# Kernel tuning notes

Hardware: AMD Instinct MI355X
Metric: run time of the kernel (lower is better)

## Reference

```python
import jax, jax.numpy as jnp
import numpy as np

DIM = 256
NUM_HEADS = 8
HEAD_DIM = DIM // NUM_HEADS
WH, WW = 7, 7
N = WH * WW              # tokens per window = 49
NUM_WINDOWS = 64         # windows per image (56x56 map / 7x7 windows)
B_TOTAL = 2048           # num_windows * B_images
SCALE = HEAD_DIM ** -0.5


def _relative_position_index():
    # Matches the tf.meshgrid (xy indexing) construction in the source.
    coords = np.stack(np.meshgrid(np.arange(WH), np.arange(WW)), axis=0)  # [2, WW, WH]
    flat = coords.reshape(2, -1)                                          # [2, N]
    rel = flat[:, :, None] - flat[:, None, :]                             # [2, N, N]
    rel = rel.transpose(1, 2, 0).astype(np.int32)                         # [N, N, 2]
    rel[:, :, 0] += WH - 1
    rel[:, :, 1] += WW - 1
    rel[:, :, 0] *= 2 * WW - 1
    return rel.sum(-1)                                                    # [N, N]


def setup_inputs() -> dict:
    key = jax.random.key(0)
    ks = jax.random.split(key, 6)
    std = 0.02
    x = jax.random.normal(ks[0], (B_TOTAL, N, DIM), dtype=jnp.float32)
    mask = jnp.zeros((NUM_WINDOWS, N, N), dtype=jnp.float32)  # 0 / -inf additive mask
    qkv_w = jax.random.normal(ks[1], (DIM, 3 * DIM), dtype=jnp.float32) * std
    qkv_b = jnp.zeros((3 * DIM,), dtype=jnp.float32)
    proj_w = jax.random.normal(ks[2], (DIM, DIM), dtype=jnp.float32) * std
    proj_b = jnp.zeros((DIM,), dtype=jnp.float32)
    n_rel = (2 * WH - 1) * (2 * WW - 1)  # 169
    bias_table = jax.random.normal(ks[3], (n_rel, NUM_HEADS), dtype=jnp.float32) * std
    rel_index = jnp.asarray(_relative_position_index(), dtype=jnp.int32)
    return {"x": x, "mask": mask, "qkv_w": qkv_w, "qkv_b": qkv_b,
            "proj_w": proj_w, "proj_b": proj_b, "bias_table": bias_table,
            "rel_index": rel_index}


def reference(x, mask, qkv_w, qkv_b, proj_w, proj_b, bias_table, rel_index):
    B = x.shape[0]
    # qkv projection -> [3, B, H, N, hd]
    qkv = x @ qkv_w + qkv_b                                  # [B, N, 3C]
    qkv = qkv.reshape(B, N, 3, NUM_HEADS, HEAD_DIM)
    qkv = jnp.transpose(qkv, (2, 0, 3, 1, 4))
    q, k, v = qkv[0], qkv[1], qkv[2]
    # scaled attention scores [B, H, N, N]
    attn = jnp.einsum('bhnd,bhmd->bhnm', q, k) * SCALE
    # relative position bias gather: [N*N] -> [N, N, H] -> [1, H, N, N]
    bias = bias_table[rel_index.reshape(-1)].reshape(N, N, NUM_HEADS)
    attn = attn + jnp.transpose(bias, (2, 0, 1))[None]
    # additive window mask [nW, N, N]
    nW = mask.shape[0]
    attn = attn.reshape(B // nW, nW, NUM_HEADS, N, N) + mask[None, :, None]
    attn = attn.reshape(B, NUM_HEADS, N, N)
    attn = jax.nn.softmax(attn, axis=-1)
    out = jnp.einsum('bhnm,bhmd->bhnd', attn, v)             # [B, H, N, hd]
    out = jnp.transpose(out, (0, 2, 1, 3)).reshape(B, N, DIM)
    return out @ proj_w + proj_b
```

## Files before the change

### kernel.cpp

```cpp
#include <hip/hip_runtime.h>

#define NTOK 49
#define NHEAD 8
#define HDIM 32
#define DIMC 256
#define SCALE_F 0.17677669529663687f

typedef __attribute__((ext_vector_type(8))) short short8;
typedef __attribute__((ext_vector_type(4))) float f32x4;

#define AS1P(p) ((__attribute__((address_space(1))) void*)(p))
#define AS3P(p) ((__attribute__((address_space(3))) void*)(p))

__device__ inline unsigned short f2bf(float f) {
    unsigned int u = __float_as_uint(f);
    u += 0x7fffu + ((u >> 16) & 1u);
    return (unsigned short)(u >> 16);
}

__global__ __launch_bounds__(256) void conv_bf16(const float* __restrict__ in,
    unsigned short* __restrict__ outp, int nv8)
{
    int i = blockIdx.x * 256 + threadIdx.x;
    if (i >= nv8) return;
    const float4* p = (const float4*)in + (size_t)i * 2;
    float4 a = p[0], b = p[1];
    union { unsigned short s[8]; uint4 v; } u;
    u.s[0] = f2bf(a.x); u.s[1] = f2bf(a.y); u.s[2] = f2bf(a.z); u.s[3] = f2bf(a.w);
    u.s[4] = f2bf(b.x); u.s[5] = f2bf(b.y); u.s[6] = f2bf(b.z); u.s[7] = f2bf(b.w);
    ((uint4*)outp)[i] = u.v;
}

__global__ __launch_bounds__(256) void pack_w(const float* __restrict__ W,
    unsigned short* __restrict__ Wp, int K, int N)
{
    int idx = blockIdx.x * 256 + threadIdx.x;
    if (idx >= K * N) return;
    int k = idx / N, n = idx - k * N;
    Wp[((size_t)(k >> 3) * N + n) * 8 + (k & 7)] = f2bf(W[idx]);
}

__global__ __launch_bounds__(256) void bm_build(const float* __restrict__ bias_table,
    const int* __restrict__ rel_index, const float* __restrict__ mask,
    float* __restrict__ bm)
{
    int idx = blockIdx.x * 256 + threadIdx.x;
    if (idx >= 64 * NHEAD * NTOK * NTOK) return;
    int wh = idx / (NTOK * NTOK);
    int ij = idx - wh * (NTOK * NTOK);
    int w = wh >> 3, h = wh & 7;
    bm[idx] = bias_table[rel_index[ij] * NHEAD + h] + mask[(size_t)w * (NTOK * NTOK) + ij];
}

template <bool OUT_BF16>
__global__ __launch_bounds__(256) void gemm_mfma(
    const unsigned short* __restrict__ A,
    const unsigned short* __restrict__ Wp,
    const float* __restrict__ Bv,
    void* __restrict__ Yv,
    int N)
{
    __shared__ __align__(16) unsigned short As[4096];
    __shared__ __align__(16) unsigned short Bs[4096];

    const int tid  = threadIdx.x;
    const int lane = tid & 63;
    const int wv   = tid >> 6;
    const int quad = lane >> 4;
    const int l15  = lane & 15;
    const long m0  = (long)blockIdx.y * 128;
    const int  n0  = blockIdx.x * 128;
    const int  wm  = (wv >> 1) * 64;
    const int  wn  = (wv & 1) * 64;

    const unsigned short* ga0 = A + (size_t)(m0 + lane) * 256 + wv * 8;
    const unsigned short* ga1 = A + (size_t)(m0 + 64 + lane) * 256 + wv * 8;
    const unsigned short* gb0 = Wp + ((size_t)wv * N + n0 + lane) * 8;
    const unsigned short* gb1 = Wp + ((size_t)wv * N + n0 + 64 + lane) * 8;

    f32x4 acc[4][4];
    #pragma unroll
    for (int i = 0; i < 4; ++i)
        #pragma unroll
        for (int j = 0; j < 4; ++j) acc[i][j] = (f32x4){0.f, 0.f, 0.f, 0.f};

    for (int k0 = 0; k0 < 256; k0 += 32) {
        const size_t bofs = (size_t)(k0 >> 3) * N * 8;
        __builtin_amdgcn_global_load_lds(AS1P(ga0 + k0),   AS3P(As + wv * 1024),       16, 0, 0);
        __builtin_amdgcn_global_load_lds(AS1P(ga1 + k0),   AS3P(As + wv * 1024 + 512), 16, 0, 0);
        __builtin_amdgcn_global_load_lds(AS1P(gb0 + bofs), AS3P(Bs + wv * 1024),       16, 0, 0);
        __builtin_amdgcn_global_load_lds(AS1P(gb1 + bofs), AS3P(Bs + wv * 1024 + 512), 16, 0, 0);
        __syncthreads();
        short8 af[4], bq[4];
        #pragma unroll
        for (int t = 0; t < 4; ++t) {
            af[t] = *(const short8*)(As + quad * 1024 + (wm + t * 16 + l15) * 8);
            bq[t] = *(const short8*)(Bs + quad * 1024 + (wn + t * 16 + l15) * 8);
        }
        #pragma unroll
        for (int ti = 0; ti < 4; ++ti)
            #pragma unroll
            for (int tj = 0; tj < 4; ++tj)
                acc[ti][tj] = __builtin_amdgcn_mfma_f32_16x16x32_bf16(af[ti], bq[tj], acc[ti][tj], 0, 0, 0);
        __syncthreads();
    }

    #pragma unroll
    for (int ti = 0; ti < 4; ++ti) {
        #pragma unroll
        for (int r = 0; r < 4; ++r) {
            const long row = m0 + wm + ti * 16 + quad * 4 + r;
            #pragma unroll
            for (int tj = 0; tj < 4; ++tj) {
                const int col = n0 + wn + tj * 16 + l15;
                float v = acc[ti][tj][r] + Bv[col];
                if (OUT_BF16) ((unsigned short*)Yv)[row * N + col] = f2bf(v);
                else          ((float*)Yv)[row * N + col] = v;
            }
        }
    }
}

__global__ __launch_bounds__(128) void attn_mfma(
    const unsigned short* __restrict__ qkvb,
    const float* __restrict__ bm,
    unsigned short* __restrict__ o1b,
    int win0)
{
    __shared__ __align__(16) unsigned short SMEM[2 * 3528];

    const int wvid = threadIdx.x >> 6;
    const int lane = threadIdx.x & 63;
    const int h    = blockIdx.x * 2 + wvid;
    const int b    = blockIdx.y;
    const int w    = (win0 + b) & 63;
    const int quad = lane >> 4;
    const int l15  = lane & 15;

    unsigned short* Vt = SMEM + wvid * 3528;
    unsigned short* Ps = SMEM + wvid * 3528;

    const unsigned short* wbase = qkvb + (size_t)b * NTOK * 768 + h * HDIM;

    {
        const int tok = (lane < NTOK) ? lane : (NTOK - 1);
        const unsigned short* vp = wbase + (size_t)tok * 768 + 512;
        #pragma unroll
        for (int c = 0; c < 4; ++c) {
            uint4 vv = *(const uint4*)(vp + c * 8);
            unsigned int uu[4] = {vv.x, vv.y, vv.z, vv.w};
            #pragma unroll
            for (int e = 0; e < 4; ++e) {
                int d = c * 8 + e * 2;
                Vt[d * 72 + lane]       = (unsigned short)(uu[e] & 0xffffu);
                Vt[(d + 1) * 72 + lane] = (unsigned short)(uu[e] >> 16);
            }
        }
    }

    short8 aq[4], bk[4];
    #pragma unroll
    for (int t = 0; t < 4; ++t) {
        int row = t * 16 + l15; if (row >= NTOK) row = NTOK - 1;
        const unsigned short* rp = wbase + (size_t)row * 768 + quad * 8;
        aq[t] = *(const short8*)(rp);
        bk[t] = *(const short8*)(rp + 256);
    }

    f32x4 sa[4][4];
    #pragma unroll
    for (int ti = 0; ti < 4; ++ti)
        #pragma unroll
        for (int tj = 0; tj < 4; ++tj) {
            f32x4 z = (f32x4){0.f, 0.f, 0.f, 0.f};
            sa[ti][tj] = __builtin_amdgcn_mfma_f32_16x16x32_bf16(aq[ti], bk[tj], z, 0, 0, 0);
        }

    short8 vb2[2][2];
    #pragma unroll
    for (int td = 0; td < 2; ++td)
        #pragma unroll
        for (int kc = 0; kc < 2; ++kc)
            vb2[td][kc] = *(const short8*)(Vt + (td * 16 + l15) * 72 + kc * 32 + quad * 8);

    const float* bmb = bm + (size_t)(w * NHEAD + h) * (NTOK * NTOK);
    float inv[4][4];
    #pragma unroll
    for (int ti = 0; ti < 4; ++ti) {
        #pragma unroll
        for (int r = 0; r < 4; ++r) {
            const int row = ti * 16 + quad * 4 + r;
            float sv[4];
            #pragma unroll
            for (int tj = 0; tj < 4; ++tj) {
                const int col = tj * 16 + l15;
                float s;
                if (col < NTOK) {
                    float add = (row < NTOK) ? bmb[row * NTOK + col] : 0.f;
                    s = sa[ti][tj][r] * SCALE_F + add;
                } else {
                    s = -__builtin_inff();
                }
                sv[tj] = s;
            }
            float mx = fmaxf(fmaxf(sv[0], sv[1]), fmaxf(sv[2], sv[3]));
            mx = fmaxf(mx, __shfl_xor(mx, 1, 16));
            mx = fmaxf(mx, __shfl_xor(mx, 2, 16));
            mx = fmaxf(mx, __shfl_xor(mx, 4, 16));
            mx = fmaxf(mx, __shfl_xor(mx, 8, 16));
            float e0 = __expf(sv[0] - mx), e1 = __expf(sv[1] - mx);
            float e2 = __expf(sv[2] - mx), e3 = __expf(sv[3] - mx);
            sa[ti][0][r] = e0; sa[ti][1][r] = e1; sa[ti][2][r] = e2; sa[ti][3][r] = e3;
            float sum = (e0 + e1) + (e2 + e3);
            sum += __shfl_xor(sum, 1, 16);
            sum += __shfl_xor(sum, 2, 16);
            sum += __shfl_xor(sum, 4, 16);
            sum += __shfl_xor(sum, 8, 16);
            inv[ti][r] = 1.f / sum;
        }
    }

    __syncthreads();

    #pragma unroll
    for (int ti = 0; ti < 4; ++ti)
        #pragma unroll
        for (int r = 0; r < 4; ++r) {
            const int row = ti * 16 + quad * 4 + r;
            if (row < NTOK) {
                #pragma unroll
                for (int tj = 0; tj < 4; ++tj)
                    Ps[row * 72 + tj * 16 + l15] = f2bf(sa[ti][tj][r]);
            }
        }

    short8 pa[4][2];
    #pragma unroll
    for (int ti = 0; ti < 4; ++ti) {
        int row = ti * 16 + l15; if (row >= NTOK) row = NTOK - 1;
        #pragma unroll
        for (int kc = 0; kc < 2; ++kc)
            pa[ti][kc] = *(const short8*)(Ps + row * 72 + kc * 32 + quad * 8);
    }
    f32x4 oa[4][2];
    #pragma unroll
    for (int ti = 0; ti < 4; ++ti)
        #pragma unroll
        for (int td = 0; td < 2; ++td) {
            f32x4 z = (f32x4){0.f, 0.f, 0.f, 0.f};
            z = __builtin_amdgcn_mfma_f32_16x16x32_bf16(pa[ti][0], vb2[td][0], z, 0, 0, 0);
            oa[ti][td] = __builtin_amdgcn_mfma_f32_16x16x32_bf16(pa[ti][1], vb2[td][1], z, 0, 0, 0);
        }

    #pragma unroll
    for (int ti = 0; ti < 4; ++ti)
        #pragma unroll
        for (int r = 0; r < 4; ++r) {
            const int row = ti * 16 + quad * 4 + r;
            if (row < NTOK) {
                const float si = inv[ti][r];
                unsigned short* op = o1b + ((size_t)b * NTOK + row) * DIMC + h * HDIM;
                #pragma unroll
                for (int td = 0; td < 2; ++td)
                    op[td * 16 + l15] = f2bf(oa[ti][td][r] * si);
            }
        }
}

extern "C" void kernel_launch(void* const* d_in, const int* in_sizes, int n_in,
                              void* d_out, int out_size, void* d_ws, size_t ws_size,
                              hipStream_t stream)
{
    const float* x          = (const float*)d_in[0];
    const float* mask       = (const float*)d_in[1];
    const float* qkv_w      = (const float*)d_in[2];
    const float* qkv_b      = (const float*)d_in[3];
    const float* proj_w     = (const float*)d_in[4];
    const float* proj_b     = (const float*)d_in[5];
    const float* bias_table = (const float*)d_in[6];
    const int*   rel_index  = (const int*)d_in[7];
    float* outp = (float*)d_out;

    const int B_TOTAL = 2048;
    char* ws = (char*)d_ws;
    size_t off = 0;
    auto carve = [&](size_t bytes) -> void* {
        void* p = ws + off; off += (bytes + 255) & ~(size_t)255; return p;
    };
    unsigned short* WpQ = (unsigned short*)carve((size_t)256 * 768 * 2);
    unsigned short* WpP = (unsigned short*)carve((size_t)256 * 256 * 2);
    float* bm = (float*)carve((size_t)64 * NHEAD * NTOK * NTOK * 4);
    const size_t fixed = off;
    const size_t PER_WIN = (size_t)NTOK * 256 * 2 + (size_t)NTOK * 768 * 2 + (size_t)NTOK * 256 * 2;
    size_t avail = (ws_size > fixed + 1024) ? (ws_size - fixed - 1024) : 0;
    int chunkW = (int)(avail / PER_WIN);
    if (chunkW > B_TOTAL) chunkW = B_TOTAL;
    chunkW &= ~127;
    if (chunkW < 128) chunkW = 128;
    unsigned short* x_bf = (unsigned short*)carve((size_t)chunkW * NTOK * 256 * 2);
    unsigned short* qkvb = (unsigned short*)carve((size_t)chunkW * NTOK * 768 * 2);
    unsigned short* o1b  = (unsigned short*)carve((size_t)chunkW * NTOK * 256 * 2);

    pack_w<<<(256 * 768 + 255) / 256, 256, 0, stream>>>(qkv_w, WpQ, 256, 768);
    pack_w<<<(256 * 256 + 255) / 256, 256, 0, stream>>>(proj_w, WpP, 256, 256);
    bm_build<<<(64 * NHEAD * NTOK * NTOK + 255) / 256, 256, 0, stream>>>(
        bias_table, rel_index, mask, bm);

    for (int w0 = 0; w0 < B_TOTAL; w0 += chunkW) {
        int wc = B_TOTAL - w0; if (wc > chunkW) wc = chunkW;
        const int Mc = wc * NTOK;
        const int nv8 = Mc * 32;
        conv_bf16<<<(nv8 + 255) / 256, 256, 0, stream>>>(
            x + (size_t)w0 * NTOK * DIMC, x_bf, nv8);
        gemm_mfma<true ><<<dim3(6, Mc / 128), 256, 0, stream>>>(x_bf, WpQ, qkv_b, qkvb, 768);
        attn_mfma<<<dim3(NHEAD / 2, wc), 128, 0, stream>>>(qkvb, bm, o1b, w0);
        gemm_mfma<false><<<dim3(2, Mc / 128), 256, 0, stream>>>(
            o1b, WpP, proj_b, outp + (size_t)w0 * NTOK * DIMC, 256);
    }
}
```

Baseline: 400.0 us.

## Pack activations k-major, swap MFMA operands for vector stores, XCD-aware block mapping

The bf16 activation buffers (x and the attention output) are now written in a k-chunk-major packed layout, the same one the weights use, so the GEMM's global-to-LDS A loads are contiguous per lane instead of 512-byte strided. The MFMA operands are swapped so each lane holds four consecutive output columns, which lets the epilogue issue float4/uint2 vector stores and load the bias as float4. The GEMM grid is flattened and remapped so each XCD works on a contiguous range of M blocks, aiming for better L2 locality. The attention kernel now writes its output with scattered 2-byte stores into the packed layout, which may cost more than the contiguous row writes it replaces.

After: 413.9 us. 1.03x slower.

```diff
diff --git a/kernel.cpp b/kernel.cpp
--- a/kernel.cpp
+++ b/kernel.cpp
@@ -18,17 +18,18 @@
     return (unsigned short)(u >> 16);
 }
 
-__global__ __launch_bounds__(256) void conv_bf16(const float* __restrict__ in,
-    unsigned short* __restrict__ outp, int nv8)
-{
-    int i = blockIdx.x * 256 + threadIdx.x;
-    if (i >= nv8) return;
-    const float4* p = (const float4*)in + (size_t)i * 2;
+__global__ __launch_bounds__(256) void conv_pack(const float* __restrict__ in,
+    unsigned short* __restrict__ xp, int M)
+{
+    const int m  = blockIdx.x * 256 + threadIdx.x;
+    const int kc = blockIdx.y;
+    if (m >= M) return;
+    const float4* p = (const float4*)(in + (size_t)m * 256 + kc * 8);
     float4 a = p[0], b = p[1];
     union { unsigned short s[8]; uint4 v; } u;
     u.s[0] = f2bf(a.x); u.s[1] = f2bf(a.y); u.s[2] = f2bf(a.z); u.s[3] = f2bf(a.w);
     u.s[4] = f2bf(b.x); u.s[5] = f2bf(b.y); u.s[6] = f2bf(b.z); u.s[7] = f2bf(b.w);
-    ((uint4*)outp)[i] = u.v;
+    *(uint4*)(xp + ((size_t)kc * M + m) * 8) = u.v;
 }
 
 __global__ __launch_bounds__(256) void pack_w(const float* __restrict__ W,
@@ -54,11 +55,11 @@
 
 template <bool OUT_BF16>
 __global__ __launch_bounds__(256) void gemm_mfma(
-    const unsigned short* __restrict__ A,
+    const unsigned short* __restrict__ Ap,
     const unsigned short* __restrict__ Wp,
     const float* __restrict__ Bv,
     void* __restrict__ Yv,
-    int N)
+    int N, int M, int nbm)
 {
     __shared__ __align__(16) unsigned short As[4096];
     __shared__ __align__(16) unsigned short Bs[4096];
@@ -68,15 +69,29 @@
     const int wv   = tid >> 6;
     const int quad = lane >> 4;
     const int l15  = lane & 15;
-    const long m0  = (long)blockIdx.y * 128;
-    const int  n0  = blockIdx.x * 128;
-    const int  wm  = (wv >> 1) * 64;
-    const int  wn  = (wv & 1) * 64;
-
-    const unsigned short* ga0 = A + (size_t)(m0 + lane) * 256 + wv * 8;
-    const unsigned short* ga1 = A + (size_t)(m0 + 64 + lane) * 256 + wv * 8;
+
+    const int nbn = N >> 7;
+    const int lin = blockIdx.x;
+    int mblk, nblk;
+    if ((nbm & 7) == 0) {
+        const int xcd = lin & 7;
+        const int g   = lin >> 3;
+        const int gm  = g / nbn;
+        mblk = xcd * (nbm >> 3) + gm;
+        nblk = g - gm * nbn;
+    } else {
+        mblk = lin / nbn;
+        nblk = lin - mblk * nbn;
+    }
+    const long m0 = (long)mblk * 128;
+    const int  n0 = nblk * 128;
+    const int  wm = (wv >> 1) * 64;
+    const int  wn = (wv & 1) * 64;
+
+    const unsigned short* ga0 = Ap + ((size_t)wv * M + m0 + lane) * 8;
+    const unsigned short* ga1 = ga0 + 64 * 8;
     const unsigned short* gb0 = Wp + ((size_t)wv * N + n0 + lane) * 8;
-    const unsigned short* gb1 = Wp + ((size_t)wv * N + n0 + 64 + lane) * 8;
+    const unsigned short* gb1 = gb0 + 64 * 8;
 
     f32x4 acc[4][4];
     #pragma unroll
@@ -85,9 +100,10 @@
         for (int j = 0; j < 4; ++j) acc[i][j] = (f32x4){0.f, 0.f, 0.f, 0.f};
 
     for (int k0 = 0; k0 < 256; k0 += 32) {
+        const size_t aofs = (size_t)(k0 >> 3) * M * 8;
         const size_t bofs = (size_t)(k0 >> 3) * N * 8;
-        __builtin_amdgcn_global_load_lds(AS1P(ga0 + k0),   AS3P(As + wv * 1024),       16, 0, 0);
-        __builtin_amdgcn_global_load_lds(AS1P(ga1 + k0),   AS3P(As + wv * 1024 + 512), 16, 0, 0);
+        __builtin_amdgcn_global_load_lds(AS1P(ga0 + aofs), AS3P(As + wv * 1024),       16, 0, 0);
+        __builtin_amdgcn_global_load_lds(AS1P(ga1 + aofs), AS3P(As + wv * 1024 + 512), 16, 0, 0);
         __builtin_amdgcn_global_load_lds(AS1P(gb0 + bofs), AS3P(Bs + wv * 1024),       16, 0, 0);
         __builtin_amdgcn_global_load_lds(AS1P(gb1 + bofs), AS3P(Bs + wv * 1024 + 512), 16, 0, 0);
         __syncthreads();
@@ -101,21 +117,33 @@
         for (int ti = 0; ti < 4; ++ti)
             #pragma unroll
             for (int tj = 0; tj < 4; ++tj)
-                acc[ti][tj] = __builtin_amdgcn_mfma_f32_16x16x32_bf16(af[ti], bq[tj], acc[ti][tj], 0, 0, 0);
+                acc[ti][tj] = __builtin_amdgcn_mfma_f32_16x16x32_bf16(bq[tj], af[ti], acc[ti][tj], 0, 0, 0);
         __syncthreads();
     }
 
+    float4 bv4[4];
+    #pragma unroll
+    for (int tj = 0; tj < 4; ++tj)
+        bv4[tj] = *(const float4*)(Bv + n0 + wn + tj * 16 + quad * 4);
+
     #pragma unroll
     for (int ti = 0; ti < 4; ++ti) {
-        #pragma unroll
-        for (int r = 0; r < 4; ++r) {
-            const long row = m0 + wm + ti * 16 + quad * 4 + r;
-            #pragma unroll
-            for (int tj = 0; tj < 4; ++tj) {
-                const int col = n0 + wn + tj * 16 + l15;
-                float v = acc[ti][tj][r] + Bv[col];
-                if (OUT_BF16) ((unsigned short*)Yv)[row * N + col] = f2bf(v);
-                else          ((float*)Yv)[row * N + col] = v;
+        const long row = m0 + wm + ti * 16 + l15;
+        #pragma unroll
+        for (int tj = 0; tj < 4; ++tj) {
+            const int col = n0 + wn + tj * 16 + quad * 4;
+            const float v0 = acc[ti][tj][0] + bv4[tj].x;
+            const float v1 = acc[ti][tj][1] + bv4[tj].y;
+            const float v2 = acc[ti][tj][2] + bv4[tj].z;
+            const float v3 = acc[ti][tj][3] + bv4[tj].w;
+            if (OUT_BF16) {
+                uint2 u;
+                u.x = (unsigned int)f2bf(v0) | ((unsigned int)f2bf(v1) << 16);
+                u.y = (unsigned int)f2bf(v2) | ((unsigned int)f2bf(v3) << 16);
+                *(uint2*)((unsigned short*)Yv + row * N + col) = u;
+            } else {
+                float4 o = {v0, v1, v2, v3};
+                *(float4*)((float*)Yv + row * N + col) = o;
             }
         }
     }
@@ -125,7 +153,7 @@
     const unsigned short* __restrict__ qkvb,
     const float* __restrict__ bm,
     unsigned short* __restrict__ o1b,
-    int win0)
+    int win0, int Mc)
 {
     __shared__ __align__(16) unsigned short SMEM[2 * 3528];
 
@@ -259,10 +287,12 @@
             const int row = ti * 16 + quad * 4 + r;
             if (row < NTOK) {
                 const float si = inv[ti][r];
-                unsigned short* op = o1b + ((size_t)b * NTOK + row) * DIMC + h * HDIM;
+                const size_t gm = (size_t)b * NTOK + row;
                 #pragma unroll
-                for (int td = 0; td < 2; ++td)
-                    op[td * 16 + l15] = f2bf(oa[ti][td][r] * si);
+                for (int td = 0; td < 2; ++td) {
+                    const int kk = h * HDIM + td * 16 + l15;
+                    o1b[((size_t)(kk >> 3) * Mc + gm) * 8 + (kk & 7)] = f2bf(oa[ti][td][r] * si);
+                }
             }
         }
 }
@@ -309,12 +339,12 @@
     for (int w0 = 0; w0 < B_TOTAL; w0 += chunkW) {
         int wc = B_TOTAL - w0; if (wc > chunkW) wc = chunkW;
         const int Mc = wc * NTOK;
-        const int nv8 = Mc * 32;
-        conv_bf16<<<(nv8 + 255) / 256, 256, 0, stream>>>(
-            x + (size_t)w0 * NTOK * DIMC, x_bf, nv8);
-        gemm_mfma<true ><<<dim3(6, Mc / 128), 256, 0, stream>>>(x_bf, WpQ, qkv_b, qkvb, 768);
-        attn_mfma<<<dim3(NHEAD / 2, wc), 128, 0, stream>>>(qkvb, bm, o1b, w0);
-        gemm_mfma<false><<<dim3(2, Mc / 128), 256, 0, stream>>>(
-            o1b, WpP, proj_b, outp + (size_t)w0 * NTOK * DIMC, 256);
-    }
-}
+        const int nbm = Mc / 128;
+        conv_pack<<<dim3((Mc + 255) / 256, 32), 256, 0, stream>>>(
+            x + (size_t)w0 * NTOK * DIMC, x_bf, Mc);
+        gemm_mfma<true ><<<dim3(nbm * 6), 256, 0, stream>>>(x_bf, WpQ, qkv_b, qkvb, 768, Mc, nbm);
+        attn_mfma<<<dim3(NHEAD / 2, wc), 128, 0, stream>>>(qkvb, bm, o1b, w0, Mc);
+        gemm_mfma<false><<<dim3(nbm * 2), 256, 0, stream>>>(
+            o1b, WpP, proj_b, outp + (size_t)w0 * NTOK * DIMC, 256, Mc, nbm);
+    }
+}
```
